# Performance work log

Hardware: AMD Instinct MI355X
Metric: run time of the kernel (lower is better)

Reference implementation:

```python
import jax, jax.numpy as jnp
import numpy as np

B, IN, OUT, K = 2048, 1024, 1024, 20


def setup_inputs() -> dict:
    key = jax.random.key(0)
    k1, k2 = jax.random.split(key)
    x = jax.random.normal(k1, (B, IN), dtype=jnp.float32)
    # per-output, per-input spline coefficients: (out_features, in_features, num_knots)
    W = jax.random.normal(k2, (OUT, IN, K), dtype=jnp.float32) * 0.1
    # evenly spaced knot grid on [-2, 2] (linspace)
    knots = jnp.linspace(-2.0, 2.0, K, dtype=jnp.float32)
    return {"x": x, "W": W, "knots": knots}


def reference(x, W, knots):
    # RBF spline basis shared across all output features (this is the fusion
    # the original per-output Python loop misses):
    # basis[b, i, k] = exp(-0.5 * ((x[b, i] - knots[k]) / h)^2)
    h = knots[1] - knots[0]  # uniform knot spacing -> RBF bandwidth
    basis = jnp.exp(-0.5 * jnp.square((x[:, :, None] - knots) / h))  # (B, IN, K)
    # Each SplineLayer o computes sum_{i,k} W[o,i,k] * basis[b,i,k]; the
    # KANBlock concatenates the OUT scalars -> a single einsum.
    return jnp.einsum("bik,oik->bo", basis, W)  # (B, OUT)
```

## Files before the change

### kernel.cpp

```cpp
#include <hip/hip_runtime.h>

#define B_DIM 2048
#define IN_DIM 1024
#define OUT_DIM 1024
#define K_KNOTS 20
#define KR (IN_DIM * K_KNOTS)
#define OUT_ELEMS (B_DIM * OUT_DIM)

#define TM 128
#define TN 128
#define BK 128
#define KSPLIT 4
#define MT_TILES (B_DIM / TM)
#define NT_TILES (OUT_DIM / TN)
#define GEMM_BLOCKS (MT_TILES * NT_TILES * KSPLIT)
#define LDS_AS0 0
#define LDS_AS1 8192
#define LDS_BS0 16384
#define LDS_BS1 24576

#define NB_QUADS (B_DIM * IN_DIM * 5)
#define NB_BASIS_BLK (NB_QUADS / 256)
#define NW4 (OUT_DIM * KR / 8)
#define NB_W_BLK (NW4 / 256)

typedef __bf16 bf16x8 __attribute__((ext_vector_type(8)));
typedef float  f32x4  __attribute__((ext_vector_type(4)));

#define MFMA16(a, b, c) __builtin_amdgcn_mfma_f32_16x16x32_bf16(a, b, c, 0, 0, 0)

__device__ __forceinline__ unsigned short f2bf(float f) {
    unsigned int u = __float_as_uint(f);
    unsigned int r = u + 0x7fffu + ((u >> 16) & 1u);
    return (unsigned short)(r >> 16);
}

__device__ __forceinline__ unsigned int pack2(float lo, float hi) {
    return (unsigned int)f2bf(lo) | ((unsigned int)f2bf(hi) << 16);
}

__device__ __forceinline__ void async_load16(const void* g, void* l) {
    __builtin_amdgcn_global_load_lds(
        (const __attribute__((address_space(1))) void*)g,
        (__attribute__((address_space(3))) void*)l,
        16, 0, 0);
}

__global__ void zero_out_kernel(float* out) {
    int idx = (blockIdx.x * 256 + threadIdx.x) * 4;
    float4 z = {0.f, 0.f, 0.f, 0.f};
    *(float4*)(out + idx) = z;
}

__global__ void __launch_bounds__(256) prep_kernel(
        const float* __restrict__ x,
        const float4* __restrict__ Wsrc,
        const float* __restrict__ knots,
        uint2* __restrict__ basis_out,
        uint4* __restrict__ w_out) {
    if (blockIdx.x < NB_BASIS_BLK) {
        unsigned int n = blockIdx.x * 256 + threadIdx.x;
        unsigned int q  = n % 5u;
        unsigned int bi = n / 5u;
        float t0 = knots[0];
        float h  = knots[1] - t0;
        float invh = 1.0f / h;
        float xv = x[bi];
        float k0 = (float)(4 * q);
        float v[4];
#pragma unroll
        for (int j = 0; j < 4; ++j) {
            float t = __builtin_fmaf(k0 + (float)j, h, t0);
            float d = (xv - t) * invh;
            v[j] = __expf(-0.5f * d * d);
        }
        uint2 o;
        o.x = pack2(v[0], v[1]);
        o.y = pack2(v[2], v[3]);
        basis_out[n] = o;
    } else {
        unsigned int t = (blockIdx.x - NB_BASIS_BLK) * 256 + threadIdx.x;
        float4 a = Wsrc[2 * t];
        float4 b = Wsrc[2 * t + 1];
        uint4 o;
        o.x = pack2(a.x, a.y);
        o.y = pack2(a.z, a.w);
        o.z = pack2(b.x, b.y);
        o.w = pack2(b.z, b.w);
        w_out[t] = o;
    }
}

#define AOFF(s, h) (((s) * 2 + (h)) * 8192)
#define BOFF(s, h) (32768 + ((s) * 2 + (h)) * 8192)

template <int KS, bool ATOMIC>
__global__ void __launch_bounds__(512, 2)
kan_gemm8(const unsigned short* __restrict__ Ab,
          const unsigned short* __restrict__ Bb,
          float* __restrict__ out) {
    __shared__ __align__(16) unsigned short lds[65536];

    constexpr int KPBk   = KR / KS;
    constexpr int NTILES = KPBk / 64;

    const int id  = blockIdx.x;
    const int z   = id & 7;
    const int ord = id >> 3;
    const int mt  = ord & 7;
    const int nt  = ord >> 3;
    const int m0  = mt * 256;
    const int n0  = nt * 256;
    const int k0  = z * KPBk;

    const int tid  = threadIdx.x;
    const int wave = tid >> 6;
    const int lane = tid & 63;
    const int wm   = wave >> 2;
    const int wn   = wave & 3;

    const int srow8 = lane >> 3;
    const int scol  = ((lane & 7) ^ srow8) * 8;

    auto stage = [&](const unsigned short* __restrict__ src, int grow, int kb, int lbase) {
        const unsigned short* g = src + (size_t)(grow + wave * 16 + srow8) * KR + kb + scol;
        async_load16(g,                  &lds[lbase + wave * 1024]);
        async_load16(g + (size_t)8 * KR, &lds[lbase + wave * 1024 + 512]);
    };

    f32x4 acc[8][4];
#pragma unroll
    for (int i = 0; i < 8; ++i)
#pragma unroll
        for (int j = 0; j < 4; ++j) acc[i][j] = (f32x4){0.f, 0.f, 0.f, 0.f};

    const int q   = lane >> 4;
    const int r15 = lane & 15;
    const int r7  = lane & 7;
    const int c0  = (q ^ r7) * 8;
    const int c1  = ((4 + q) ^ r7) * 8;

    stage(Ab, m0,       k0,      AOFF(0, 0));
    stage(Ab, m0 + 128, k0,      AOFF(0, 1));
    stage(Bb, n0,       k0,      BOFF(0, 0));
    stage(Bb, n0 + 128, k0,      BOFF(0, 1));
    stage(Bb, n0,       k0 + 64, BOFF(1, 0));
    stage(Ab, m0,       k0 + 64, AOFF(1, 0));
    asm volatile("s_waitcnt vmcnt(4)" ::: "memory");
    __builtin_amdgcn_s_barrier();

#pragma unroll 2
    for (int t = 0; t < NTILES; ++t) {
        const int s   = t & 1;
        const int aB  = s * 16384 + (wm * 128 + r15) * 64;
        const int bB  = 32768 + s * 16384 + (wn * 64 + r15) * 64;
        const int kb1 = k0 + (t + 1) * 64;
        const int kb2 = k0 + (t + 2) * 64;
        bf16x8 aR[4][2], bR[4][2];

#pragma unroll
        for (int i = 0; i < 4; ++i) {
            aR[i][0] = *(const bf16x8*)&lds[aB + i * 1024 + c0];
            aR[i][1] = *(const bf16x8*)&lds[aB + i * 1024 + c1];
        }
#pragma unroll
        for (int j = 0; j < 2; ++j) {
            bR[j][0] = *(const bf16x8*)&lds[bB + j * 1024 + c0];
            bR[j][1] = *(const bf16x8*)&lds[bB + j * 1024 + c1];
        }
        if (t + 1 < NTILES) stage(Bb, n0 + 128, kb1, BOFF(s ^ 1, 1));
        __builtin_amdgcn_s_barrier();
        asm volatile("s_waitcnt lgkmcnt(0)" ::: "memory");
        __builtin_amdgcn_sched_barrier(0);
        __builtin_amdgcn_s_setprio(1);
#pragma unroll
        for (int i = 0; i < 4; ++i)
#pragma unroll
            for (int j = 0; j < 2; ++j) {
                acc[i][j] = MFMA16(aR[i][0], bR[j][0], acc[i][j]);
                acc[i][j] = MFMA16(aR[i][1], bR[j][1], acc[i][j]);
            }
        __builtin_amdgcn_s_setprio(0);
        __builtin_amdgcn_s_barrier();

#pragma unroll
        for (int j = 2; j < 4; ++j) {
            bR[j][0] = *(const bf16x8*)&lds[bB + j * 1024 + c0];
            bR[j][1] = *(const bf16x8*)&lds[bB + j * 1024 + c1];
        }
        if (t + 1 < NTILES) stage(Ab, m0 + 128, kb1, AOFF(s ^ 1, 1));
        __builtin_amdgcn_s_barrier();
        asm volatile("s_waitcnt lgkmcnt(0)" ::: "memory");
        __builtin_amdgcn_sched_barrier(0);
        __builtin_amdgcn_s_setprio(1);
#pragma unroll
        for (int i = 0; i < 4; ++i)
#pragma unroll
            for (int j = 2; j < 4; ++j) {
                acc[i][j] = MFMA16(aR[i][0], bR[j][0], acc[i][j]);
                acc[i][j] = MFMA16(aR[i][1], bR[j][1], acc[i][j]);
            }
        __builtin_amdgcn_s_setprio(0);
        __builtin_amdgcn_s_barrier();

#pragma unroll
        for (int i = 0; i < 4; ++i) {
            aR[i][0] = *(const bf16x8*)&lds[aB + (4 + i) * 1024 + c0];
            aR[i][1] = *(const bf16x8*)&lds[aB + (4 + i) * 1024 + c1];
        }
        if (t + 2 < NTILES) stage(Bb, n0, kb2, BOFF(s, 0));
        __builtin_amdgcn_s_barrier();
        asm volatile("s_waitcnt lgkmcnt(0)" ::: "memory");
        __builtin_amdgcn_sched_barrier(0);
        __builtin_amdgcn_s_setprio(1);
#pragma unroll
        for (int i = 0; i < 4; ++i)
#pragma unroll
            for (int j = 2; j < 4; ++j) {
                acc[4 + i][j] = MFMA16(aR[i][0], bR[j][0], acc[4 + i][j]);
                acc[4 + i][j] = MFMA16(aR[i][1], bR[j][1], acc[4 + i][j]);
            }
        __builtin_amdgcn_s_setprio(0);
        __builtin_amdgcn_s_barrier();

        if (t + 2 < NTILES) stage(Ab, m0, kb2, AOFF(s, 0));
        __builtin_amdgcn_s_setprio(1);
#pragma unroll
        for (int i = 0; i < 4; ++i)
#pragma unroll
            for (int j = 0; j < 2; ++j) {
                acc[4 + i][j] = MFMA16(aR[i][0], bR[j][0], acc[4 + i][j]);
                acc[4 + i][j] = MFMA16(aR[i][1], bR[j][1], acc[4 + i][j]);
            }
        __builtin_amdgcn_s_setprio(0);
        if (t < NTILES - 2) asm volatile("s_waitcnt vmcnt(4)" ::: "memory");
        else                asm volatile("s_waitcnt vmcnt(0)" ::: "memory");
        __builtin_amdgcn_s_barrier();
    }

    float* dst = ATOMIC ? out : out + (size_t)z * OUT_ELEMS;
#pragma unroll
    for (int i = 0; i < 8; ++i)
#pragma unroll
        for (int j = 0; j < 4; ++j)
#pragma unroll
            for (int r = 0; r < 4; ++r) {
                const int row = m0 + wm * 128 + i * 16 + q * 4 + r;
                const int c   = n0 + wn * 64  + j * 16 + r15;
                if (ATOMIC)
                    atomicAdd(&dst[(size_t)row * OUT_DIM + c], acc[i][j][r]);
                else
                    dst[(size_t)row * OUT_DIM + c] = acc[i][j][r];
            }
}

template <int KS, bool ATOMIC>
__global__ void __launch_bounds__(256)
kan_gemm(const unsigned short* __restrict__ Ab,
         const unsigned short* __restrict__ Bb,
         float* __restrict__ out) {
    __shared__ __align__(16) unsigned short lds[32768];

    const int KPBk = KR / KS;
    const int id   = blockIdx.x;
    const int xcd  = id & 7;
    const int ord  = id >> 3;
    const int mt   = xcd * 2 + (ord & 1);
    const int nt   = (ord >> 1) & (NT_TILES - 1);
    const int z    = ord >> 4;
    const int m0 = mt * TM;
    const int n0 = nt * TN;
    const int k0 = z * KPBk;

    const int tid  = threadIdx.x;
    const int wave = tid >> 6;
    const int lane = tid & 63;
    const int wm = wave & 1;
    const int wn = wave >> 1;

    const int srow = lane >> 3;
    const int scol = ((lane & 7) ^ srow) * 8;

    f32x4 acc[4][4];
#pragma unroll
    for (int i = 0; i < 4; ++i)
#pragma unroll
        for (int j = 0; j < 4; ++j) acc[i][j] = (f32x4){0.f, 0.f, 0.f, 0.f};

    for (int kt = 0; kt < KPBk; kt += BK) {
        const int kb = k0 + kt;
        __syncthreads();
#pragma unroll
        for (int c = 0; c < 4; ++c) {
            const int chunk = wave * 4 + c;
            const int r = chunk * 8 + srow;
            const unsigned short* arow = Ab + (size_t)(m0 + r) * KR + kb + scol;
            const unsigned short* brow = Bb + (size_t)(n0 + r) * KR + kb + scol;
            unsigned short* slot = &lds[chunk * 512];
            async_load16(arow,      slot + LDS_AS0);
            async_load16(arow + 64, slot + LDS_AS1);
            async_load16(brow,      slot + LDS_BS0);
            async_load16(brow + 64, slot + LDS_BS1);
        }
        __syncthreads();

        const int quad = lane >> 4;
        const int r15  = lane & 15;
        const int r7   = lane & 7;
#pragma unroll
        for (int s = 0; s < 4; ++s) {
            const int abase = (s >> 1) ? LDS_AS1 : LDS_AS0;
            const int bbase = (s >> 1) ? LDS_BS1 : LDS_BS0;
            const int cg = (s & 1) * 4 + quad;
            const int xo = (cg ^ r7) * 8;
            bf16x8 af[4], bfv[4];
#pragma unroll
            for (int i = 0; i < 4; ++i) {
                af[i]  = *(const bf16x8*)&lds[abase + (wm * 64 + i * 16 + r15) * 64 + xo];
                bfv[i] = *(const bf16x8*)&lds[bbase + (wn * 64 + i * 16 + r15) * 64 + xo];
            }
#pragma unroll
            for (int i = 0; i < 4; ++i)
#pragma unroll
                for (int j = 0; j < 4; ++j)
                    acc[i][j] = MFMA16(af[i], bfv[j], acc[i][j]);
        }
    }

    float* dst = ATOMIC ? out : out + (size_t)z * OUT_ELEMS;
    const int quad = lane >> 4;
    const int col  = lane & 15;
#pragma unroll
    for (int i = 0; i < 4; ++i)
#pragma unroll
        for (int j = 0; j < 4; ++j)
#pragma unroll
            for (int r = 0; r < 4; ++r) {
                const int row = m0 + wm * 64 + i * 16 + quad * 4 + r;
                const int c   = n0 + wn * 64 + j * 16 + col;
                if (ATOMIC)
                    atomicAdd(&dst[(size_t)row * OUT_DIM + c], acc[i][j][r]);
                else
                    dst[(size_t)row * OUT_DIM + c] = acc[i][j][r];
            }
}

template <int KS>
__global__ void kan_reduce(const float* __restrict__ part, float* __restrict__ out) {
    const int idx = (blockIdx.x * 256 + threadIdx.x) * 4;
    f32x4 s = *(const f32x4*)(part + idx);
#pragma unroll
    for (int z = 1; z < KS; ++z)
        s += *(const f32x4*)(part + (size_t)z * OUT_ELEMS + idx);
    *(f32x4*)(out + idx) = s;
}

__global__ void kan_fallback(const float* __restrict__ x,
                             const float* __restrict__ W,
                             const float* __restrict__ knots,
                             float* __restrict__ out) {
    __shared__ float basis[256 * K_KNOTS];
    const int b = blockIdx.x;
    const int o = blockIdx.y * blockDim.x + threadIdx.x;
    const float invh = 1.0f / (knots[1] - knots[0]);
    const float* w = W + (size_t)o * KR;
    float sum = 0.f;
    for (int i0 = 0; i0 < IN_DIM; i0 += 256) {
        __syncthreads();
        for (int idx = threadIdx.x; idx < 256 * K_KNOTS; idx += blockDim.x) {
            const int i = i0 + idx / K_KNOTS;
            const int k = idx % K_KNOTS;
            const float d = (x[(size_t)b * IN_DIM + i] - knots[k]) * invh;
            basis[idx] = __expf(-0.5f * d * d);
        }
        __syncthreads();
        for (int r = 0; r < 256 * K_KNOTS; ++r)
            sum += basis[r] * w[(size_t)i0 * K_KNOTS + r];
    }
    out[(size_t)b * OUT_DIM + o] = sum;
}

extern "C" void kernel_launch(void* const* d_in, const int* in_sizes, int n_in,
                              void* d_out, int out_size, void* d_ws, size_t ws_size,
                              hipStream_t stream) {
    const float* x     = (const float*)d_in[0];
    const float* W     = (const float*)d_in[1];
    const float* knots = (const float*)d_in[2];
    float* out = (float*)d_out;

    const size_t basis_bytes = (size_t)B_DIM * KR * 2;
    const size_t wb_bytes    = (size_t)OUT_DIM * KR * 2;
    const size_t part8_bytes = (size_t)8 * OUT_ELEMS * 4;
    const size_t part4_bytes = (size_t)4 * OUT_ELEMS * 4;

    unsigned short* Ab = (unsigned short*)d_ws;
    unsigned short* Bb = (unsigned short*)((char*)d_ws + basis_bytes);
    float* part = (float*)((char*)d_ws + basis_bytes + wb_bytes);

    if (ws_size >= basis_bytes + wb_bytes + part8_bytes) {
        prep_kernel<<<dim3(NB_BASIS_BLK + NB_W_BLK), dim3(256), 0, stream>>>(
            x, (const float4*)W, knots, (uint2*)Ab, (uint4*)Bb);
        kan_gemm8<8, false><<<dim3(256), dim3(512), 0, stream>>>(Ab, Bb, part);
        kan_reduce<8><<<dim3(OUT_ELEMS / (256 * 4)), dim3(256), 0, stream>>>(part, out);
    } else if (ws_size >= basis_bytes + wb_bytes + part4_bytes) {
        prep_kernel<<<dim3(NB_BASIS_BLK + NB_W_BLK), dim3(256), 0, stream>>>(
            x, (const float4*)W, knots, (uint2*)Ab, (uint4*)Bb);
        kan_gemm<4, false><<<dim3(GEMM_BLOCKS), dim3(256), 0, stream>>>(Ab, Bb, part);
        kan_reduce<4><<<dim3(OUT_ELEMS / (256 * 4)), dim3(256), 0, stream>>>(part, out);
    } else if (ws_size >= basis_bytes + wb_bytes) {
        zero_out_kernel<<<dim3(OUT_ELEMS / (256 * 4)), dim3(256), 0, stream>>>(out);
        prep_kernel<<<dim3(NB_BASIS_BLK + NB_W_BLK), dim3(256), 0, stream>>>(
            x, (const float4*)W, knots, (uint2*)Ab, (uint4*)Bb);
        kan_gemm8<8, true><<<dim3(256), dim3(512), 0, stream>>>(Ab, Bb, out);
    } else {
        kan_fallback<<<dim3(B_DIM, OUT_DIM / 256), dim3(256), 0, stream>>>(x, W, knots, out);
    }
}
```

Measured before the change: 250.4 us.

## Restructure GEMM main loop with fewer barriers and partial LDS waits

Rewrites the bf16 MFMA GEMM K-loop as a templated per-stage step. The four barrier-separated phases become one phase with a single mid-step barrier, and both prefetch pairs are issued together. LDS fragment reads are issued ahead and waited on with partial lgkmcnt counts, so MFMAs can start before all reads land. This cuts workgroup barriers and exposed LDS latency, but holds more live registers (an extra A fragment set) and depends on subtle cross-wave ordering of LDS buffer reuse. The loop also assumes the tile count is even.

Measured after the change: 257.3 us. 1.03x slower.

```diff
diff --git a/kernel.cpp b/kernel.cpp
--- a/kernel.cpp
+++ b/kernel.cpp
@@ -94,6 +94,116 @@
 #define AOFF(s, h) (((s) * 2 + (h)) * 8192)
 #define BOFF(s, h) (32768 + ((s) * 2 + (h)) * 8192)
 
+template <int S>
+__device__ __forceinline__ void tile_step(
+        int t, int ntiles,
+        const unsigned short* __restrict__ Ab,
+        const unsigned short* __restrict__ Bb,
+        unsigned short* lds,
+        f32x4 (&acc)[8][4],
+        int m0, int n0, int k0,
+        int wave, int wm, int wn, int r15, int c0, int c1,
+        int srow8, int scol) {
+    const int aB  = S * 16384 + (wm * 128 + r15) * 64;
+    const int bB  = 32768 + S * 16384 + (wn * 64 + r15) * 64;
+    const int kb1 = k0 + (t + 1) * 64;
+    const int kb2 = k0 + (t + 2) * 64;
+
+    auto stage = [&](const unsigned short* __restrict__ src, int grow, int kb, int lbase) {
+        const unsigned short* g = src + (size_t)(grow + wave * 16 + srow8) * KR + kb + scol;
+        async_load16(g,                  &lds[lbase + wave * 1024]);
+        async_load16(g + (size_t)8 * KR, &lds[lbase + wave * 1024 + 512]);
+    };
+
+    if (t + 1 < ntiles) {
+        stage(Bb, n0 + 128, kb1, BOFF(S ^ 1, 1));
+        stage(Ab, m0 + 128, kb1, AOFF(S ^ 1, 1));
+    }
+
+    bf16x8 aR[4][2], bR[4][2], aS[4][2];
+#pragma unroll
+    for (int i = 0; i < 4; ++i) {
+        aR[i][0] = *(const bf16x8*)&lds[aB + i * 1024 + c0];
+        aR[i][1] = *(const bf16x8*)&lds[aB + i * 1024 + c1];
+    }
+#pragma unroll
+    for (int j = 0; j < 2; ++j) {
+        bR[j][0] = *(const bf16x8*)&lds[bB + j * 1024 + c0];
+        bR[j][1] = *(const bf16x8*)&lds[bB + j * 1024 + c1];
+    }
+#pragma unroll
+    for (int j = 2; j < 4; ++j) {
+        bR[j][0] = *(const bf16x8*)&lds[bB + j * 1024 + c0];
+        bR[j][1] = *(const bf16x8*)&lds[bB + j * 1024 + c1];
+    }
+#pragma unroll
+    for (int i = 0; i < 2; ++i) {
+        aS[i][0] = *(const bf16x8*)&lds[aB + (4 + i) * 1024 + c0];
+        aS[i][1] = *(const bf16x8*)&lds[aB + (4 + i) * 1024 + c1];
+    }
+
+    asm volatile("s_waitcnt lgkmcnt(8)" ::: "memory");
+    __builtin_amdgcn_sched_barrier(0);
+    __builtin_amdgcn_s_setprio(1);
+#pragma unroll
+    for (int i = 0; i < 4; ++i)
+#pragma unroll
+        for (int j = 0; j < 2; ++j) {
+            acc[i][j] = MFMA16(aR[i][0], bR[j][0], acc[i][j]);
+            acc[i][j] = MFMA16(aR[i][1], bR[j][1], acc[i][j]);
+        }
+    __builtin_amdgcn_s_setprio(0);
+
+#pragma unroll
+    for (int i = 2; i < 4; ++i) {
+        aS[i][0] = *(const bf16x8*)&lds[aB + (4 + i) * 1024 + c0];
+        aS[i][1] = *(const bf16x8*)&lds[aB + (4 + i) * 1024 + c1];
+    }
+
+    asm volatile("s_waitcnt lgkmcnt(4)" ::: "memory");
+    __builtin_amdgcn_sched_barrier(0);
+    __builtin_amdgcn_s_setprio(1);
+#pragma unroll
+    for (int i = 0; i < 4; ++i)
+#pragma unroll
+        for (int j = 2; j < 4; ++j) {
+            acc[i][j] = MFMA16(aR[i][0], bR[j][0], acc[i][j]);
+            acc[i][j] = MFMA16(aR[i][1], bR[j][1], acc[i][j]);
+        }
+    __builtin_amdgcn_s_setprio(0);
+
+    asm volatile("s_waitcnt lgkmcnt(0)" ::: "memory");
+    __builtin_amdgcn_sched_barrier(0);
+    __builtin_amdgcn_s_barrier();
+    __builtin_amdgcn_sched_barrier(0);
+
+    if (t + 2 < ntiles) {
+        stage(Bb, n0, kb2, BOFF(S, 0));
+        stage(Ab, m0, kb2, AOFF(S, 0));
+    }
+
+    __builtin_amdgcn_s_setprio(1);
+#pragma unroll
+    for (int i = 0; i < 4; ++i)
+#pragma unroll
+        for (int j = 2; j < 4; ++j) {
+            acc[4 + i][j] = MFMA16(aS[i][0], bR[j][0], acc[4 + i][j]);
+            acc[4 + i][j] = MFMA16(aS[i][1], bR[j][1], acc[4 + i][j]);
+        }
+#pragma unroll
+    for (int i = 0; i < 4; ++i)
+#pragma unroll
+        for (int j = 0; j < 2; ++j) {
+            acc[4 + i][j] = MFMA16(aS[i][0], bR[j][0], acc[4 + i][j]);
+            acc[4 + i][j] = MFMA16(aS[i][1], bR[j][1], acc[4 + i][j]);
+        }
+    __builtin_amdgcn_s_setprio(0);
+
+    if (t < ntiles - 2) asm volatile("s_waitcnt vmcnt(4)" ::: "memory");
+    else                asm volatile("s_waitcnt vmcnt(0)" ::: "memory");
+    __builtin_amdgcn_s_barrier();
+}
+
 template <int KS, bool ATOMIC>
 __global__ void __launch_bounds__(512, 2)
 kan_gemm8(const unsigned short* __restrict__ Ab,
@@ -149,93 +259,11 @@
     asm volatile("s_waitcnt vmcnt(4)" ::: "memory");
     __builtin_amdgcn_s_barrier();
 
-#pragma unroll 2
-    for (int t = 0; t < NTILES; ++t) {
-        const int s   = t & 1;
-        const int aB  = s * 16384 + (wm * 128 + r15) * 64;
-        const int bB  = 32768 + s * 16384 + (wn * 64 + r15) * 64;
-        const int kb1 = k0 + (t + 1) * 64;
-        const int kb2 = k0 + (t + 2) * 64;
-        bf16x8 aR[4][2], bR[4][2];
-
-#pragma unroll
-        for (int i = 0; i < 4; ++i) {
-            aR[i][0] = *(const bf16x8*)&lds[aB + i * 1024 + c0];
-            aR[i][1] = *(const bf16x8*)&lds[aB + i * 1024 + c1];
-        }
-#pragma unroll
-        for (int j = 0; j < 2; ++j) {
-            bR[j][0] = *(const bf16x8*)&lds[bB + j * 1024 + c0];
-            bR[j][1] = *(const bf16x8*)&lds[bB + j * 1024 + c1];
-        }
-        if (t + 1 < NTILES) stage(Bb, n0 + 128, kb1, BOFF(s ^ 1, 1));
-        __builtin_amdgcn_s_barrier();
-        asm volatile("s_waitcnt lgkmcnt(0)" ::: "memory");
-        __builtin_amdgcn_sched_barrier(0);
-        __builtin_amdgcn_s_setprio(1);
-#pragma unroll
-        for (int i = 0; i < 4; ++i)
-#pragma unroll
-            for (int j = 0; j < 2; ++j) {
-                acc[i][j] = MFMA16(aR[i][0], bR[j][0], acc[i][j]);
-                acc[i][j] = MFMA16(aR[i][1], bR[j][1], acc[i][j]);
-            }
-        __builtin_amdgcn_s_setprio(0);
-        __builtin_amdgcn_s_barrier();
-
-#pragma unroll
-        for (int j = 2; j < 4; ++j) {
-            bR[j][0] = *(const bf16x8*)&lds[bB + j * 1024 + c0];
-            bR[j][1] = *(const bf16x8*)&lds[bB + j * 1024 + c1];
-        }
-        if (t + 1 < NTILES) stage(Ab, m0 + 128, kb1, AOFF(s ^ 1, 1));
-        __builtin_amdgcn_s_barrier();
-        asm volatile("s_waitcnt lgkmcnt(0)" ::: "memory");
-        __builtin_amdgcn_sched_barrier(0);
-        __builtin_amdgcn_s_setprio(1);
-#pragma unroll
-        for (int i = 0; i < 4; ++i)
-#pragma unroll
-            for (int j = 2; j < 4; ++j) {
-                acc[i][j] = MFMA16(aR[i][0], bR[j][0], acc[i][j]);
-                acc[i][j] = MFMA16(aR[i][1], bR[j][1], acc[i][j]);
-            }
-        __builtin_amdgcn_s_setprio(0);
-        __builtin_amdgcn_s_barrier();
-
-#pragma unroll
-        for (int i = 0; i < 4; ++i) {
-            aR[i][0] = *(const bf16x8*)&lds[aB + (4 + i) * 1024 + c0];
-            aR[i][1] = *(const bf16x8*)&lds[aB + (4 + i) * 1024 + c1];
-        }
-        if (t + 2 < NTILES) stage(Bb, n0, kb2, BOFF(s, 0));
-        __builtin_amdgcn_s_barrier();
-        asm volatile("s_waitcnt lgkmcnt(0)" ::: "memory");
-        __builtin_amdgcn_sched_barrier(0);
-        __builtin_amdgcn_s_setprio(1);
-#pragma unroll
-        for (int i = 0; i < 4; ++i)
-#pragma unroll
-            for (int j = 2; j < 4; ++j) {
-                acc[4 + i][j] = MFMA16(aR[i][0], bR[j][0], acc[4 + i][j]);
-                acc[4 + i][j] = MFMA16(aR[i][1], bR[j][1], acc[4 + i][j]);
-            }
-        __builtin_amdgcn_s_setprio(0);
-        __builtin_amdgcn_s_barrier();
-
-        if (t + 2 < NTILES) stage(Ab, m0, kb2, AOFF(s, 0));
-        __builtin_amdgcn_s_setprio(1);
-#pragma unroll
-        for (int i = 0; i < 4; ++i)
-#pragma unroll
-            for (int j = 0; j < 2; ++j) {
-                acc[4 + i][j] = MFMA16(aR[i][0], bR[j][0], acc[4 + i][j]);
-                acc[4 + i][j] = MFMA16(aR[i][1], bR[j][1], acc[4 + i][j]);
-            }
-        __builtin_amdgcn_s_setprio(0);
-        if (t < NTILES - 2) asm volatile("s_waitcnt vmcnt(4)" ::: "memory");
-        else                asm volatile("s_waitcnt vmcnt(0)" ::: "memory");
-        __builtin_amdgcn_s_barrier();
+    for (int tt = 0; tt < NTILES; tt += 2) {
+        tile_step<0>(tt,     NTILES, Ab, Bb, lds, acc, m0, n0, k0,
+                     wave, wm, wn, r15, c0, c1, srow8, scol);
+        tile_step<1>(tt + 1, NTILES, Ab, Bb, lds, acc, m0, n0, k0,
+                     wave, wm, wn, r15, c0, c1, srow8, scol);
     }
 
     float* dst = ATOMIC ? out : out + (size_t)z * OUT_ELEMS;
```
